# Performance work log

Hardware: AMD Instinct MI355X
Metric: run time of the kernel (lower is better)

Reference implementation:

```python
import jax, jax.numpy as jnp
from jax import lax
import numpy as np

B, CIN, COUT, T, H, W, KH, KW = 8, 256, 256, 16, 28, 28, 3, 3


def setup_inputs() -> dict:
    key = jax.random.key(0)
    k1, k2, k3 = jax.random.split(key, 3)
    x = jax.random.normal(k1, (B, CIN, T, H, W), dtype=jnp.float32)
    alpha = jax.random.uniform(k2, (B, CIN, T, 1, 1), dtype=jnp.float32)
    # base weight, kaiming-uniform-like init, stored as [1,1,c_out,c_in,kh,kw]
    fan_in = CIN * KH * KW
    bound = 1.0 / np.sqrt(fan_in)
    weight = jax.random.uniform(k3, (1, 1, COUT, CIN, KH, KW), dtype=jnp.float32,
                                minval=-bound, maxval=bound)
    return {"x": x, "alpha": alpha, "weight": weight}


def reference(x, alpha, weight):
    # x: [b, c_in, t, h, w]; alpha: [b, c_in, t, 1, 1]; weight: [1,1,c_out,c_in,kh,kw]
    b, c_in, t, h, w = x.shape
    c_out = weight.shape[2]
    w_base = weight[0, 0]  # [c_out, c_in, kh, kw]
    # W_t = alpha_t * W_base scales only input channels (alpha broadcasts over c_out),
    # so (alpha*W) conv x == W conv (alpha*x): modulate input, then one shared conv.
    xm = x * alpha  # [b, c_in, t, h, w]
    xm = jnp.transpose(xm, (0, 2, 1, 3, 4)).reshape(b * t, c_in, h, w)
    y = lax.conv_general_dilated(
        xm, w_base,
        window_strides=(1, 1),
        padding=((1, 1), (1, 1)),
        dimension_numbers=("NCHW", "OIHW", "NCHW"),
    )  # [b*t, c_out, h, w]
    oh, ow = y.shape[-2], y.shape[-1]
    y = y.reshape(b, t, c_out, oh, ow)
    return jnp.transpose(y, (0, 2, 1, 3, 4))  # [b, c_out, t, h, w]
```

## Files before the change

kernel.cpp:

```cpp
#include <hip/hip_runtime.h>
#include <hip/hip_bf16.h>
#include <cstdint>

#define CIN   256
#define COUT  256
#define NB    8
#define NT    16
#define NH    28
#define NW    28
#define HP    30
#define WP    30

#define XM_ELEMS   ((size_t)NB * NT * HP * WP * CIN)
#define XM_BYTES   (XM_ELEMS * 2)

typedef __bf16 bf16x8 __attribute__((ext_vector_type(8)));
typedef float  f32x4  __attribute__((ext_vector_type(4)));

#define AS1 __attribute__((address_space(1)))
#define AS3 __attribute__((address_space(3)))

static __device__ __forceinline__ unsigned short f2bf(float f) {
    __hip_bfloat16 h = __float2bfloat16(f);
    return __builtin_bit_cast(unsigned short, h);
}

__global__ void modulate_kernel(const float* __restrict__ x,
                                const float* __restrict__ alpha,
                                unsigned short* __restrict__ xm) {
    const int ci = threadIdx.x;
    const int blk = blockIdx.x;
    const int hp = blk % 30;
    const int bt = blk / 30;
    unsigned short* row = xm + (size_t)(bt * 900 + hp * 30) * 256;
    if (hp == 0 || hp == 29) {
        #pragma unroll
        for (int wp = 0; wp < 30; ++wp) row[wp * 256 + ci] = 0;
        return;
    }
    const int t = bt & 15, b = bt >> 4;
    const int h = hp - 1;
    const float a = alpha[(b * CIN + ci) * NT + t];
    const float* xrow = x + ((size_t)((b * CIN + ci) * NT + t) * NH + h) * NW;
    row[ci] = 0;
    row[29 * 256 + ci] = 0;
    const float4* xv = (const float4*)xrow;
    #pragma unroll
    for (int q = 0; q < 7; ++q) {
        float4 v = xv[q];
        row[(q * 4 + 1) * 256 + ci] = f2bf(v.x * a);
        row[(q * 4 + 2) * 256 + ci] = f2bf(v.y * a);
        row[(q * 4 + 3) * 256 + ci] = f2bf(v.z * a);
        row[(q * 4 + 4) * 256 + ci] = f2bf(v.w * a);
    }
}

__global__ void repack_w_kernel(const float* __restrict__ w,
                                unsigned short* __restrict__ wB) {
    const int ci = threadIdx.x;
    const int tap = blockIdx.x >> 8;
    const int co  = blockIdx.x & 255;
    wB[((tap * 256 + co) * 256) + ci] = f2bf(w[(co * 256 + ci) * 9 + tap]);
}


#define BAR()    __builtin_amdgcn_s_barrier()
#define LGKM0()  asm volatile("s_waitcnt lgkmcnt(0)" ::: "memory")
#define VMW(N)   asm volatile("s_waitcnt vmcnt(" #N ")" ::: "memory")
#define SCHED0() __builtin_amdgcn_sched_barrier(0)
#define PRIO(x)  __builtin_amdgcn_s_setprio(x)

#define STAGE(P, aOffE, bOffE) do {                                           \
    _Pragma("unroll") for (int a_ = 0; a_ < 4; ++a_)                          \
        __builtin_amdgcn_global_load_lds(                                     \
            (const AS1 void*)(aSrcLane + (aOffE) + a_ * 4096),                \
            (AS3 void*)(lds + (P)*16384 + (wv*4 + a_)*1024 + lane*16),        \
            16, 0, 0);                                                        \
    _Pragma("unroll") for (int b_ = 0; b_ < 2; ++b_)                          \
        __builtin_amdgcn_global_load_lds(                                     \
            (const AS1 void*)(bL[b_] + (bOffE)),                              \
            (AS3 void*)(lds + 32768 + (P)*8192 + (wv*2 + b_)*1024 + lane*16), \
            16, 0, 0);                                                        \
} while (0)

#define STAGE_NEXT(P) do {                                                    \
    const int kh2 = (tap2 * 11) >> 5;                                         \
    const int kw2 = tap2 - 3 * kh2;                                           \
    STAGE(P, tap2 * 65536 + cic2 * 32,                                        \
             ((kh2 - 1) * 30 + (kw2 - 1)) * 256 + cic2 * 32);                 \
    if (++tap2 == 9) { tap2 = 0; ++cic2; }                                    \
} while (0)

#define READF(SET, P) do {                                                    \
    _Pragma("unroll") for (int m_ = 0; m_ < 4; ++m_)                          \
        fa##SET[m_] = *(const bf16x8*)(lds + (P)*16384 + aRdBase + m_*1024);  \
    _Pragma("unroll") for (int f_ = 0; f_ < 7; ++f_)                          \
        fb##SET[f_] = *(const bf16x8*)(lds + 32768 + (P)*8192 + bRdBase + f_*1024);\
} while (0)

#define MFMA28(SET) do {                                                      \
    _Pragma("unroll") for (int m_ = 0; m_ < 4; ++m_)                          \
    _Pragma("unroll") for (int f_ = 0; f_ < 7; ++f_)                          \
        acc[m_][f_] = __builtin_amdgcn_mfma_f32_16x16x32_bf16(                \
            fb##SET[f_], fa##SET[m_], acc[m_][f_], 0, 0, 0);                  \
} while (0)

__global__ __launch_bounds__(256, 2) void conv_gemm_kernel(
    const unsigned short* __restrict__ xm,
    const unsigned short* __restrict__ wB,
    float* __restrict__ out) {
    __shared__ __align__(1024) char lds[49152];

    const int tid  = threadIdx.x;
    const int wv   = tid >> 6;
    const int lane = tid & 63;
    const int l15  = lane & 15;
    const int n0   = blockIdx.x * 112;

    const int swzE = 8 * ((lane & 3) ^ ((lane >> 3) & 3));
    const unsigned short* aSrcLane = wB + (wv * 64 + (lane >> 2)) * 256 + swzE;

    const unsigned short* bL[2];
    #pragma unroll
    for (int b_ = 0; b_ < 2; ++b_) {
        int nl = wv * 32 + b_ * 16 + (lane >> 2);
        nl = nl > 111 ? 111 : nl;
        const int n  = n0 + nl;
        const int w_ = n % 28, h_ = (n / 28) % 28, bt = n / 784;
        bL[b_] = xm + (size_t)((bt * 30 + h_ + 1) * 30 + (w_ + 1)) * 256 + swzE;
    }

    const int readSwz = ((lane >> 4) ^ ((l15 >> 1) & 3)) << 4;
    const int aRdBase = wv * 4096 + l15 * 64 + readSwz;
    const int bRdBase = l15 * 64 + readSwz;

    f32x4 acc[4][7];
    #pragma unroll
    for (int i = 0; i < 4; ++i)
        #pragma unroll
        for (int j = 0; j < 7; ++j) acc[i][j] = f32x4{0.f, 0.f, 0.f, 0.f};

    bf16x8 faA[4], fbA[7], faB[4], fbB[7];

    int tap2 = 0, cic2 = 0;
    STAGE_NEXT(0);
    STAGE_NEXT(1);
    VMW(6);
    SCHED0();
    BAR();
    READF(A, 0);
    LGKM0();

    #pragma unroll 1
    for (int kt = 0; kt < 70; kt += 2) {
        VMW(0);
        SCHED0();
        BAR();
        READF(B, 1);
        STAGE_NEXT(0);
        SCHED0();
        PRIO(1); MFMA28(A); PRIO(0);
        LGKM0();
        VMW(0);
        SCHED0();
        BAR();
        READF(A, 0);
        STAGE_NEXT(1);
        SCHED0();
        PRIO(1); MFMA28(B); PRIO(0);
        LGKM0();
    }
    VMW(0);
    SCHED0();
    BAR();
    READF(B, 1);
    SCHED0();
    PRIO(1); MFMA28(A); PRIO(0);
    LGKM0();
    PRIO(1); MFMA28(B); PRIO(0);

    #pragma unroll
    for (int f = 0; f < 7; ++f) {
        const int n  = n0 + f * 16 + ((lane >> 4) << 2);
        const int bt = n / 784;
        const int hw = n - bt * 784;
        const int b = bt >> 4, t = bt & 15;
        float* obase = out + ((size_t)(b * 256) * 16 + t) * 784 + hw;
        #pragma unroll
        for (int m = 0; m < 4; ++m) {
            const int co = wv * 64 + m * 16 + l15;
            *(f32x4*)(obase + (size_t)co * 12544) = acc[m][f];
        }
    }
}

extern "C" void kernel_launch(void* const* d_in, const int* in_sizes, int n_in,
                              void* d_out, int out_size, void* d_ws, size_t ws_size,
                              hipStream_t stream) {
    const float* x      = (const float*)d_in[0];
    const float* alpha  = (const float*)d_in[1];
    const float* weight = (const float*)d_in[2];
    float* out = (float*)d_out;

    unsigned short* xm = (unsigned short*)d_ws;
    unsigned short* wB = (unsigned short*)((char*)d_ws + XM_BYTES);

    modulate_kernel<<<dim3(NB * NT * HP), dim3(256), 0, stream>>>(x, alpha, xm);
    repack_w_kernel<<<dim3(9 * 256), dim3(256), 0, stream>>>(weight, wB);
    conv_gemm_kernel<<<dim3(896), dim3(256), 0, stream>>>(xm, wB, out);
}
```

Before: 173.4 us.

## Enlarge GEMM block tile to 256x224 with 8 waves in 4x2 grid

```diff
diff --git a/kernel.cpp b/kernel.cpp
--- a/kernel.cpp
+++ b/kernel.cpp
@@ -70,69 +70,68 @@
 #define SCHED0() __builtin_amdgcn_sched_barrier(0)
 #define PRIO(x)  __builtin_amdgcn_s_setprio(x)
 
-#define STAGE(P, aOffE, bOffE) do {                                           \
-    _Pragma("unroll") for (int a_ = 0; a_ < 4; ++a_)                          \
-        __builtin_amdgcn_global_load_lds(                                     \
-            (const AS1 void*)(aSrcLane + (aOffE) + a_ * 4096),                \
-            (AS3 void*)(lds + (P)*16384 + (wv*4 + a_)*1024 + lane*16),        \
-            16, 0, 0);                                                        \
-    _Pragma("unroll") for (int b_ = 0; b_ < 2; ++b_)                          \
-        __builtin_amdgcn_global_load_lds(                                     \
-            (const AS1 void*)(bL[b_] + (bOffE)),                              \
-            (AS3 void*)(lds + 32768 + (P)*8192 + (wv*2 + b_)*1024 + lane*16), \
-            16, 0, 0);                                                        \
-} while (0)
-
-#define STAGE_NEXT(P) do {                                                    \
+#define STAGE_F(P) do {                                                       \
     const int kh2 = (tap2 * 11) >> 5;                                         \
     const int kw2 = tap2 - 3 * kh2;                                           \
-    STAGE(P, tap2 * 65536 + cic2 * 32,                                        \
-             ((kh2 - 1) * 30 + (kw2 - 1)) * 256 + cic2 * 32);                 \
+    const int aOff = tap2 * 65536 + cic2 * 32;                                \
+    const int bOff = ((kh2 - 1) * 30 + (kw2 - 1)) * 256 + cic2 * 32;          \
+    _Pragma("unroll") for (int c_ = 0; c_ < 2; ++c_)                          \
+        __builtin_amdgcn_global_load_lds(                                     \
+            (const AS1 void*)(aSrc + aOff + c_ * 32768),                      \
+            (AS3 void*)(lds + (P)*32768 + (c_*128 + wave*16)*64 + lane*16),   \
+            16, 0, 0);                                                        \
+    _Pragma("unroll") for (int c_ = 0; c_ < 2; ++c_)                          \
+        __builtin_amdgcn_global_load_lds(                                     \
+            (const AS1 void*)(bL[c_] + bOff),                                 \
+            (AS3 void*)(lds + (P)*32768 + 16384 + (c_*128 + wave*16)*64 + lane*16), \
+            16, 0, 0);                                                        \
     if (++tap2 == 9) { tap2 = 0; ++cic2; }                                    \
 } while (0)
 
-#define READF(SET, P) do {                                                    \
+#define READF(S, P) do {                                                      \
     _Pragma("unroll") for (int m_ = 0; m_ < 4; ++m_)                          \
-        fa##SET[m_] = *(const bf16x8*)(lds + (P)*16384 + aRdBase + m_*1024);  \
+        fa##S[m_] = *(const bf16x8*)(lds + (P)*32768 +                        \
+            (wm*64 + m_*16 + l15)*64 + readSwz);                              \
     _Pragma("unroll") for (int f_ = 0; f_ < 7; ++f_)                          \
-        fb##SET[f_] = *(const bf16x8*)(lds + 32768 + (P)*8192 + bRdBase + f_*1024);\
+        fb##S[f_] = *(const bf16x8*)(lds + (P)*32768 + 16384 +                \
+            (wn*112 + f_*16 + l15)*64 + readSwz);                             \
 } while (0)
 
-#define MFMA28(SET) do {                                                      \
+#define MFMA28(S) do {                                                        \
     _Pragma("unroll") for (int m_ = 0; m_ < 4; ++m_)                          \
     _Pragma("unroll") for (int f_ = 0; f_ < 7; ++f_)                          \
         acc[m_][f_] = __builtin_amdgcn_mfma_f32_16x16x32_bf16(                \
-            fb##SET[f_], fa##SET[m_], acc[m_][f_], 0, 0, 0);                  \
+            fb##S[f_], fa##S[m_], acc[m_][f_], 0, 0, 0);                      \
 } while (0)
 
-__global__ __launch_bounds__(256, 2) void conv_gemm_kernel(
+__global__ __launch_bounds__(512, 2) void conv_gemm_kernel(
     const unsigned short* __restrict__ xm,
     const unsigned short* __restrict__ wB,
     float* __restrict__ out) {
-    __shared__ __align__(1024) char lds[49152];
+    __shared__ __align__(1024) char lds[65536];
 
     const int tid  = threadIdx.x;
-    const int wv   = tid >> 6;
+    const int wave = tid >> 6;
     const int lane = tid & 63;
     const int l15  = lane & 15;
-    const int n0   = blockIdx.x * 112;
+    const int n0   = blockIdx.x * 224;
+    const int wm   = wave >> 1;
+    const int wn   = wave & 1;
 
     const int swzE = 8 * ((lane & 3) ^ ((lane >> 3) & 3));
-    const unsigned short* aSrcLane = wB + (wv * 64 + (lane >> 2)) * 256 + swzE;
+    const unsigned short* aSrc = wB + (wave * 16 + (lane >> 2)) * 256 + swzE;
 
     const unsigned short* bL[2];
     #pragma unroll
-    for (int b_ = 0; b_ < 2; ++b_) {
-        int nl = wv * 32 + b_ * 16 + (lane >> 2);
-        nl = nl > 111 ? 111 : nl;
+    for (int c_ = 0; c_ < 2; ++c_) {
+        int nl = c_ * 128 + wave * 16 + (lane >> 2);
+        nl = nl > 223 ? 223 : nl;
         const int n  = n0 + nl;
         const int w_ = n % 28, h_ = (n / 28) % 28, bt = n / 784;
-        bL[b_] = xm + (size_t)((bt * 30 + h_ + 1) * 30 + (w_ + 1)) * 256 + swzE;
+        bL[c_] = xm + (size_t)((bt * 30 + h_ + 1) * 30 + (w_ + 1)) * 256 + swzE;
     }
 
     const int readSwz = ((lane >> 4) ^ ((l15 >> 1) & 3)) << 4;
-    const int aRdBase = wv * 4096 + l15 * 64 + readSwz;
-    const int bRdBase = l15 * 64 + readSwz;
 
     f32x4 acc[4][7];
     #pragma unroll
@@ -143,32 +142,34 @@
     bf16x8 faA[4], fbA[7], faB[4], fbB[7];
 
     int tap2 = 0, cic2 = 0;
-    STAGE_NEXT(0);
-    STAGE_NEXT(1);
-    VMW(6);
+    STAGE_F(0);
+    STAGE_F(1);
+    VMW(4);
     SCHED0();
     BAR();
     READF(A, 0);
     LGKM0();
 
     #pragma unroll 1
-    for (int kt = 0; kt < 70; kt += 2) {
+    for (int it = 0; it < 35; ++it) {
         VMW(0);
         SCHED0();
         BAR();
         READF(B, 1);
-        STAGE_NEXT(0);
+        STAGE_F(0);
         SCHED0();
         PRIO(1); MFMA28(A); PRIO(0);
         LGKM0();
+        SCHED0();
         VMW(0);
         SCHED0();
         BAR();
         READF(A, 0);
-        STAGE_NEXT(1);
+        STAGE_F(1);
         SCHED0();
         PRIO(1); MFMA28(B); PRIO(0);
         LGKM0();
+        SCHED0();
     }
     VMW(0);
     SCHED0();
@@ -177,18 +178,19 @@
     SCHED0();
     PRIO(1); MFMA28(A); PRIO(0);
     LGKM0();
+    SCHED0();
     PRIO(1); MFMA28(B); PRIO(0);
 
     #pragma unroll
     for (int f = 0; f < 7; ++f) {
-        const int n  = n0 + f * 16 + ((lane >> 4) << 2);
+        const int n  = n0 + wn * 112 + f * 16 + ((lane >> 4) << 2);
         const int bt = n / 784;
         const int hw = n - bt * 784;
         const int b = bt >> 4, t = bt & 15;
         float* obase = out + ((size_t)(b * 256) * 16 + t) * 784 + hw;
         #pragma unroll
         for (int m = 0; m < 4; ++m) {
-            const int co = wv * 64 + m * 16 + l15;
+            const int co = wm * 64 + m * 16 + l15;
             *(f32x4*)(obase + (size_t)co * 12544) = acc[m][f];
         }
     }
@@ -207,5 +209,5 @@
 
     modulate_kernel<<<dim3(NB * NT * HP), dim3(256), 0, stream>>>(x, alpha, xm);
     repack_w_kernel<<<dim3(9 * 256), dim3(256), 0, stream>>>(weight, wB);
-    conv_gemm_kernel<<<dim3(896), dim3(256), 0, stream>>>(xm, wB, out);
-}
+    conv_gemm_kernel<<<dim3(448), dim3(512), 0, stream>>>(xm, wB, out);
+}
```

Result: faster. 167.0 us (-3.7%).
